# Kernel tuning notes

Measured on AMD Instinct MI355X. Metric: run time of the kernel, lower is better.

The kernel has to match this reference:

```python
import jax, jax.numpy as jnp
import numpy as np


def setup_inputs() -> dict:
    key = jax.random.key(0)
    k1, k2, k3, k4, k5 = jax.random.split(key, 5)
    num_chunks, input_dim, output_dim = 100000, 256, 512
    num_members, num_cells = 400000, 50000
    chunk_features = jax.random.normal(k1, (num_chunks, input_dim), dtype=jnp.float32)
    member_idx = jax.random.randint(k2, (num_members,), 0, num_chunks, dtype=jnp.int32)
    segment_ids = jnp.sort(jax.random.randint(k3, (num_members,), 0, num_cells, dtype=jnp.int32))
    W = jax.random.normal(k4, (input_dim, output_dim), dtype=jnp.float32) / np.sqrt(input_dim)
    b = jax.random.normal(k5, (output_dim,), dtype=jnp.float32) * 0.01
    return {
        "chunk_features": chunk_features,
        "member_idx": member_idx,
        "segment_ids": segment_ids,
        "num_cells": num_cells,
        "W": W,
        "b": b,
    }


def reference(chunk_features, member_idx, segment_ids, num_cells, W, b):
    # Gather per-membership chunk embeddings: (M, D)
    gathered = jnp.take(chunk_features, member_idx, axis=0)
    # Segment-sum over cells, then divide by counts -> segment mean (num_cells, D)
    sums = jax.ops.segment_sum(gathered, segment_ids, num_segments=num_cells)
    counts = jax.ops.segment_sum(
        jnp.ones((member_idx.shape[0],), dtype=chunk_features.dtype),
        segment_ids, num_segments=num_cells)
    cell_emb = sums / jnp.maximum(counts, 1.0)[:, None]
    # Linear projection (input_dim != output_dim)
    return cell_emb @ W + b
```

## Files before the change

### kernel.cpp

```cpp
#include <hip/hip_runtime.h>

typedef __attribute__((ext_vector_type(8))) short short8;
typedef __attribute__((ext_vector_type(4))) unsigned short ushort4v;
typedef __attribute__((ext_vector_type(4))) float floatx4;

static __device__ __forceinline__ unsigned short f2bf(float f) {
    unsigned int u = __float_as_uint(f);
    u = (u + 0x7FFFu + ((u >> 16) & 1u)) >> 16;
    return (unsigned short)u;
}

__global__ __launch_bounds__(256) void prep_kernel(
        const int* __restrict__ seg, int M, int num_cells,
        const float* __restrict__ W,
        int* __restrict__ starts,
        unsigned short* __restrict__ Wt,
        int startB) {
    const int b = blockIdx.x;
    const int tid = threadIdx.x;
    if (b < startB) {
        int m = b * 256 + tid;
        if (m > M) return;
        int prev = (m == 0) ? -1 : seg[m - 1];
        int cur  = (m == M) ? num_cells : seg[m];
        for (int c = prev + 1; c <= cur; ++c) starts[c] = m;
    } else {
        int g = (b - startB) * 256 + tid;
        if (g < 512 * 256) {
            int n = g >> 8, k = g & 255;
            Wt[g] = f2bf(W[k * 512 + n]);
        }
    }
}

__global__ __launch_bounds__(256) void seg_mean_kernel(
        const float* __restrict__ cf,
        const int* __restrict__ member_idx,
        const int* __restrict__ starts,
        int num_cells,
        unsigned short* __restrict__ cell_emb) {
    const int wid  = threadIdx.x >> 6;
    const int lane = threadIdx.x & 63;
    const int c = blockIdx.x * 4 + wid;

    float acc[4] = {0.f, 0.f, 0.f, 0.f};
    int cnt = 0;

    if (c < num_cells) {
        const int s = starts[c];
        const int e = starts[c + 1];
        cnt = e - s;

        for (int base = s; base < e; base += 64) {
            int m = base + lane;
            int idx = (m < e) ? member_idx[m] : 0;
            int n = e - base; if (n > 64) n = 64;
            for (int j0 = 0; j0 < n; j0 += 8) {
                float4 v[8];
#pragma unroll
                for (int p = 0; p < 8; ++p) {
                    int j = j0 + p;
                    if (j < n) {
                        int ci = __shfl(idx, j);
                        v[p] = *(const float4*)(cf + (size_t)ci * 256 + lane * 4);
                    }
                }
#pragma unroll
                for (int p = 0; p < 8; ++p) {
                    int j = j0 + p;
                    if (j < n) {
                        acc[0] += v[p].x; acc[1] += v[p].y;
                        acc[2] += v[p].z; acc[3] += v[p].w;
                    }
                }
            }
        }
    }

    float inv = (cnt > 0) ? 1.0f / (float)cnt : 0.f;
    ushort4v o;
#pragma unroll
    for (int t = 0; t < 4; ++t) o[t] = f2bf(acc[t] * inv);
    *(ushort4v*)(cell_emb + (size_t)c * 256 + lane * 4) = o;
}

__global__ __launch_bounds__(256) void gemm_kernel(
        const unsigned short* __restrict__ A,
        const unsigned short* __restrict__ Bt,
        const float* __restrict__ bias,
        float* __restrict__ out,
        int Mreal) {
    constexpr int LDSS = 40;
    __shared__ unsigned short As[128 * LDSS];
    __shared__ unsigned short Bs[128 * LDSS];

    const int tid  = threadIdx.x;
    const int wid  = tid >> 6;
    const int lane = tid & 63;
    const int wm = wid & 1, wn = wid >> 1;
    const int l15 = lane & 15, q = lane >> 4;
    const int m0 = blockIdx.y * 128;
    const int n0 = blockIdx.x * 128;

    floatx4 acc[4][4] = {};

    for (int kb = 0; kb < 256; kb += 32) {
#pragma unroll
        for (int r = 0; r < 2; ++r) {
            int chunk = tid + r * 256;
            int row = chunk >> 2;
            int col = (chunk & 3) * 8;
            *(short8*)&As[row * LDSS + col] =
                *(const short8*)&A[(size_t)(m0 + row) * 256 + kb + col];
            *(short8*)&Bs[row * LDSS + col] =
                *(const short8*)&Bt[(size_t)(n0 + row) * 256 + kb + col];
        }
        __syncthreads();

        short8 af[4], bf[4];
#pragma unroll
        for (int mi = 0; mi < 4; ++mi)
            af[mi] = *(const short8*)&As[(wm * 64 + mi * 16 + l15) * LDSS + q * 8];
#pragma unroll
        for (int ni = 0; ni < 4; ++ni)
            bf[ni] = *(const short8*)&Bs[(wn * 64 + ni * 16 + l15) * LDSS + q * 8];
#pragma unroll
        for (int mi = 0; mi < 4; ++mi)
#pragma unroll
            for (int ni = 0; ni < 4; ++ni)
                acc[mi][ni] = __builtin_amdgcn_mfma_f32_16x16x32_bf16(
                    af[mi], bf[ni], acc[mi][ni], 0, 0, 0);
        __syncthreads();
    }

#pragma unroll
    for (int ni = 0; ni < 4; ++ni) {
        int n = n0 + wn * 64 + ni * 16 + l15;
        float bv = bias[n];
#pragma unroll
        for (int mi = 0; mi < 4; ++mi) {
            int mbase = m0 + wm * 64 + mi * 16 + q * 4;
#pragma unroll
            for (int r = 0; r < 4; ++r) {
                int row = mbase + r;
                if (row < Mreal)
                    out[(size_t)row * 512 + n] = acc[mi][ni][r] + bv;
            }
        }
    }
}

extern "C" void kernel_launch(void* const* d_in, const int* in_sizes, int n_in,
                              void* d_out, int out_size, void* d_ws, size_t ws_size,
                              hipStream_t stream) {
    const float* chunk_features = (const float*)d_in[0];
    const int*   member_idx     = (const int*)d_in[1];
    const int*   segment_ids    = (const int*)d_in[2];
    const float* W              = (const float*)d_in[4];
    const float* bias           = (const float*)d_in[5];
    float* out = (float*)d_out;

    const int M          = in_sizes[1];
    const int out_dim    = in_sizes[5];
    const int num_cells  = out_size / out_dim;
    const int mtiles = (num_cells + 127) / 128;
    const int Mpad   = mtiles * 128;

    unsigned short* cell_emb = (unsigned short*)d_ws;
    unsigned short* Wt       = cell_emb + (size_t)Mpad * 256;
    int*            starts   = (int*)(Wt + 512 * 256);

    const int startB = (M + 1 + 255) / 256;
    const int wtB    = (512 * 256 + 255) / 256;

    hipLaunchKernelGGL(prep_kernel, dim3(startB + wtB), dim3(256), 0, stream,
                       segment_ids, M, num_cells, W, starts, Wt, startB);
    hipLaunchKernelGGL(seg_mean_kernel, dim3(Mpad / 4), dim3(256), 0, stream,
                       chunk_features, member_idx, starts, num_cells, cell_emb);
    hipLaunchKernelGGL(gemm_kernel, dim3(4, mtiles), dim3(256), 0, stream,
                       cell_emb, Wt, bias, out, num_cells);
}
```

Before: 278.6 us.

## Widen GEMM tile to 128x256 with 8 waves and XCD-aware block remap

The GEMM now uses 512-thread blocks that each compute a 128x256 output tile, so every A tile loaded into LDS is reused across twice as many output columns. The grid drops to 2 column blocks per row tile. Block indices are remapped so that consecutive work-group ids land on the same XCD, with the aim of sharing the A rows in that XCD's L2. The cost is fewer blocks and more LDS per block, which may lower occupancy.

```diff
diff --git a/kernel.cpp b/kernel.cpp
--- a/kernel.cpp
+++ b/kernel.cpp
@@ -84,34 +84,45 @@
     *(ushort4v*)(cell_emb + (size_t)c * 256 + lane * 4) = o;
 }
 
-__global__ __launch_bounds__(256) void gemm_kernel(
+__global__ __launch_bounds__(512) void gemm_kernel(
         const unsigned short* __restrict__ A,
         const unsigned short* __restrict__ Bt,
         const float* __restrict__ bias,
         float* __restrict__ out,
-        int Mreal) {
+        int Mreal, int nwgy) {
     constexpr int LDSS = 40;
     __shared__ unsigned short As[128 * LDSS];
-    __shared__ unsigned short Bs[128 * LDSS];
+    __shared__ unsigned short Bs[256 * LDSS];
+
+    const int lin = blockIdx.y * 2 + blockIdx.x;
+    const int nwg = nwgy * 2;
+    const int q = nwg >> 3, r = nwg & 7;
+    const int xcd = lin & 7, off = lin >> 3;
+    const int wgid = (xcd < r ? xcd * (q + 1) : r * (q + 1) + (xcd - r) * q) + off;
+    const int by = wgid >> 1, bx = wgid & 1;
 
     const int tid  = threadIdx.x;
     const int wid  = tid >> 6;
     const int lane = tid & 63;
     const int wm = wid & 1, wn = wid >> 1;
-    const int l15 = lane & 15, q = lane >> 4;
-    const int m0 = blockIdx.y * 128;
-    const int n0 = blockIdx.x * 128;
+    const int l15 = lane & 15, qq = lane >> 4;
+    const int m0 = by * 128;
+    const int n0 = bx * 256;
 
     floatx4 acc[4][4] = {};
 
     for (int kb = 0; kb < 256; kb += 32) {
+        {
+            int row = tid >> 2;
+            int col = (tid & 3) * 8;
+            *(short8*)&As[row * LDSS + col] =
+                *(const short8*)&A[(size_t)(m0 + row) * 256 + kb + col];
+        }
 #pragma unroll
-        for (int r = 0; r < 2; ++r) {
-            int chunk = tid + r * 256;
+        for (int rr = 0; rr < 2; ++rr) {
+            int chunk = tid + rr * 512;
             int row = chunk >> 2;
             int col = (chunk & 3) * 8;
-            *(short8*)&As[row * LDSS + col] =
-                *(const short8*)&A[(size_t)(m0 + row) * 256 + kb + col];
             *(short8*)&Bs[row * LDSS + col] =
                 *(const short8*)&Bt[(size_t)(n0 + row) * 256 + kb + col];
         }
@@ -120,10 +131,10 @@
         short8 af[4], bf[4];
 #pragma unroll
         for (int mi = 0; mi < 4; ++mi)
-            af[mi] = *(const short8*)&As[(wm * 64 + mi * 16 + l15) * LDSS + q * 8];
+            af[mi] = *(const short8*)&As[(wm * 64 + mi * 16 + l15) * LDSS + qq * 8];
 #pragma unroll
         for (int ni = 0; ni < 4; ++ni)
-            bf[ni] = *(const short8*)&Bs[(wn * 64 + ni * 16 + l15) * LDSS + q * 8];
+            bf[ni] = *(const short8*)&Bs[(wn * 64 + ni * 16 + l15) * LDSS + qq * 8];
 #pragma unroll
         for (int mi = 0; mi < 4; ++mi)
 #pragma unroll
@@ -139,12 +150,12 @@
         float bv = bias[n];
 #pragma unroll
         for (int mi = 0; mi < 4; ++mi) {
-            int mbase = m0 + wm * 64 + mi * 16 + q * 4;
+            int mbase = m0 + wm * 64 + mi * 16 + qq * 4;
 #pragma unroll
-            for (int r = 0; r < 4; ++r) {
-                int row = mbase + r;
+            for (int rr = 0; rr < 4; ++rr) {
+                int row = mbase + rr;
                 if (row < Mreal)
-                    out[(size_t)row * 512 + n] = acc[mi][ni][r] + bv;
+                    out[(size_t)row * 512 + n] = acc[mi][ni][rr] + bv;
             }
         }
     }
@@ -177,6 +188,6 @@
                        segment_ids, M, num_cells, W, starts, Wt, startB);
     hipLaunchKernelGGL(seg_mean_kernel, dim3(Mpad / 4), dim3(256), 0, stream,
                        chunk_features, member_idx, starts, num_cells, cell_emb);
-    hipLaunchKernelGGL(gemm_kernel, dim3(4, mtiles), dim3(256), 0, stream,
-                       cell_emb, Wt, bias, out, num_cells);
+    hipLaunchKernelGGL(gemm_kernel, dim3(2, mtiles), dim3(512), 0, stream,
+                       cell_emb, Wt, bias, out, num_cells, mtiles);
 }
```

New measurement: 278.7 us. About the same (+0.1%).
